# Kernel tuning notes

Measured on AMD Instinct MI355X. Metric: run time of the kernel, lower is better.

## Reference

```python
import jax, jax.numpy as jnp
import numpy as np

# Model dims
B, N, T = 2, 32, 256
D_MODEL = 128          # d_slow
D_STATE = 16
N_LAYERS = 2
EXPAND = 2
D_INNER = EXPAND * D_MODEL   # 256
D_CONV = 4
DT_RANK = (D_MODEL + 15) // 16  # 8


def setup_inputs() -> dict:
    key = jax.random.key(0)
    ks = jax.random.split(key, 8)
    s = lambda k, shape, scale: jax.random.normal(k, shape, jnp.float32) * scale
    return {
        "x": jax.random.normal(ks[0], (B, N, T, D_MODEL), jnp.float32),
        "in_proj_w": s(ks[1], (N_LAYERS, D_MODEL, 2 * D_INNER), 0.05),
        "conv_w": s(ks[2], (N_LAYERS, D_INNER, 1, D_CONV), 0.2),   # depthwise conv kernels
        "conv_b": jnp.zeros((N_LAYERS, D_INNER), jnp.float32),
        "x_proj_w": s(ks[3], (N_LAYERS, D_INNER, DT_RANK + 2 * D_STATE), 0.05),
        "dt_proj_w": s(ks[4], (N_LAYERS, DT_RANK, D_INNER), 0.1),
        "dt_proj_b": jnp.full((N_LAYERS, D_INNER), -4.0, jnp.float32),  # softplus(-4) ~ small dt
        # slow-timescale init: A_log = log(U(0.001, 0.1)) so A = -exp(A_log) is a weak decay
        "A_log": jnp.log(jax.random.uniform(ks[5], (N_LAYERS, D_INNER, D_STATE),
                                            minval=1e-3, maxval=0.1)),
        "D_param": jnp.ones((N_LAYERS, D_INNER), jnp.float32),
        "out_proj_w": s(ks[6], (N_LAYERS, D_INNER, D_MODEL), 0.05),
    }


def _selective_scan(u, delta, A, Bm, Cm, Dp):
    # u, delta: [b, t, d]; A: [d, n]; Bm, Cm: [b, t, n]; Dp: [d]
    deltaA = jnp.exp(jnp.einsum('btd,dn->btdn', delta, A))          # [b,t,d,n]
    deltaBu = jnp.einsum('btd,btn->btdn', delta * u, Bm)            # [b,t,d,n]
    # time-major for scan
    dA_t = jnp.transpose(deltaA, (1, 0, 2, 3))
    dBu_t = jnp.transpose(deltaBu, (1, 0, 2, 3))
    c_t = jnp.transpose(Cm, (1, 0, 2))

    def step(h, xs):
        dA, dBu, c = xs
        h = dA * h + dBu                                            # [b,d,n]
        y = jnp.einsum('bdn,bn->bd', h, c)
        return h, y

    h0 = jnp.zeros(u.shape[:1] + (u.shape[-1], A.shape[-1]), u.dtype)
    _, ys = jax.lax.scan(step, h0, (dA_t, dBu_t, c_t))              # ys: [t,b,d]
    y = jnp.transpose(ys, (1, 0, 2))
    return y + u * Dp


def _mamba_block(h, in_w, cw, cb, xw, dtw, dtb, A_log, Dp, ow):
    # h: [b, t, d_model]
    xz = h @ in_w                                                   # [b,t,2*d_inner]
    u, res = jnp.split(xz, 2, axis=-1)
    # causal depthwise conv over time
    u_nch = jnp.transpose(u, (0, 2, 1))                             # [b,d_inner,t]
    u_conv = jax.lax.conv_general_dilated(
        u_nch, cw, window_strides=(1,), padding=[(D_CONV - 1, 0)],
        dimension_numbers=('NCH', 'OIH', 'NCH'), feature_group_count=D_INNER)
    u = jax.nn.silu(jnp.transpose(u_conv + cb[None, :, None], (0, 2, 1)))
    # input-dependent dt, B, C
    dbl = u @ xw                                                    # [b,t,dt_rank+2n]
    dt, Bm, Cm = jnp.split(dbl, [DT_RANK, DT_RANK + D_STATE], axis=-1)
    delta = jax.nn.softplus(dt @ dtw + dtb)                         # [b,t,d_inner]
    A = -jnp.exp(A_log)                                             # [d_inner, n]
    y = _selective_scan(u, delta, A, Bm, Cm, Dp)
    return (y * jax.nn.silu(res)) @ ow


def reference(x, in_proj_w, conv_w, conv_b, x_proj_w, dt_proj_w, dt_proj_b,
              A_log, D_param, out_proj_w):
    b, n, t, d = x.shape
    h = x.reshape(b * n, t, d)
    for l in range(N_LAYERS):
        h = _mamba_block(h, in_proj_w[l], conv_w[l], conv_b[l], x_proj_w[l],
                         dt_proj_w[l], dt_proj_b[l], A_log[l], D_param[l],
                         out_proj_w[l])
    return h.reshape(b, n, t, d)
```

## Files before the change

kernel.cpp:

```cpp
#include <hip/hip_runtime.h>
#include <math.h>

#define BT 64
#define T 256
#define DM 128
#define DI 256
#define DS 16
#define DR 8
#define M_ROWS (BT*T)
#define NC 16
#define CL (T/NC)

typedef __attribute__((ext_vector_type(8))) short short8v;
typedef __attribute__((ext_vector_type(4))) float f32x4;
typedef __attribute__((ext_vector_type(4))) unsigned int uint4v;
union U8 { unsigned int u[4]; uint4v v; short8v s; };

__device__ __forceinline__ float fast_silu(float x) {
  return x * __builtin_amdgcn_rcpf(1.0f + __expf(-x));
}
__device__ __forceinline__ float softplus_f(float x) {
  return fmaxf(x, 0.0f) + __logf(1.0f + __expf(-fabsf(x)));
}

__device__ __forceinline__ void split3(const float* x, short8v& o1, short8v& o2, short8v& o3) {
  unsigned int h1[8], h2[8], h3[8];
#pragma unroll
  for (int e = 0; e < 8; e++) {
    const float xe = x[e];
    const unsigned int a = __float_as_uint(xe) & 0xFFFF0000u;
    const float r1 = xe - __uint_as_float(a);
    const unsigned int b = __float_as_uint(r1) & 0xFFFF0000u;
    const float r2 = r1 - __uint_as_float(b);
    const unsigned int c = __float_as_uint(r2) & 0xFFFF0000u;
    h1[e] = a; h2[e] = b; h3[e] = c;
  }
  U8 u1, u2, u3;
#pragma unroll
  for (int q = 0; q < 4; q++) {
    u1.u[q] = (h1[2 * q] >> 16) | (h1[2 * q + 1] & 0xFFFF0000u);
    u2.u[q] = (h2[2 * q] >> 16) | (h2[2 * q + 1] & 0xFFFF0000u);
    u3.u[q] = (h3[2 * q] >> 16) | (h3[2 * q + 1] & 0xFFFF0000u);
  }
  o1 = u1.s; o2 = u2.s; o3 = u3.s;
}

__global__ __launch_bounds__(64) void prep_all(
    const float* __restrict__ in_w, const float* __restrict__ xw,
    const float* __restrict__ dtw, const float* __restrict__ ow,
    unsigned int* __restrict__ pw1, unsigned int* __restrict__ pwb,
    unsigned int* __restrict__ pow_) {
  const int b = blockIdx.x;
  const int l = threadIdx.x;
  const int rA = l & 15, kg = l >> 4;
  float x[8];
  unsigned int* dst;
  size_t base;
  if (b < 256) {
    const int layer = b >> 7, rem = b & 127;
    const int ks = rem >> 5, cf = rem & 31;
    const int col = cf * 16 + rA, k0 = ks * 32 + kg * 8;
    const float* W = in_w + (size_t)layer * 128 * 512;
#pragma unroll
    for (int e = 0; e < 8; e++) x[e] = W[(size_t)(k0 + e) * 512 + col];
    dst = pw1 + (size_t)layer * 98304;
    base = (((size_t)ks * 32 + cf) * 64 + l) * 4;
    short8v p1, p2, p3; split3(x, p1, p2, p3);
    U8 t;
    t.s = p1; *reinterpret_cast<uint4v*>(dst + base) = t.v;
    t.s = p2; *reinterpret_cast<uint4v*>(dst + 32768 + base) = t.v;
    t.s = p3; *reinterpret_cast<uint4v*>(dst + 65536 + base) = t.v;
  } else if (b < 576) {
    const int bb = b - 256;
    const int layer = bb / 160, rem = bb % 160;
    const int ks = rem / 20, cf = rem % 20;
    const int col = cf * 16 + rA, k0 = ks * 32 + kg * 8;
    const float* xwl = xw + (size_t)layer * DI * 40;
    const float* dtwl = dtw + (size_t)layer * DR * DI;
#pragma unroll
    for (int e = 0; e < 8; e++) {
      const int k = k0 + e;
      float v = 0.f;
      if (col < 256) {
#pragma unroll
        for (int r = 0; r < DR; r++) v += xwl[k * 40 + r] * dtwl[r * DI + col];
      } else if (col < 288) {
        v = xwl[k * 40 + 8 + (col - 256)];
      }
      x[e] = v;
    }
    dst = pwb + (size_t)layer * 122880;
    base = (((size_t)ks * 20 + cf) * 64 + l) * 4;
    short8v p1, p2, p3; split3(x, p1, p2, p3);
    U8 t;
    t.s = p1; *reinterpret_cast<uint4v*>(dst + base) = t.v;
    t.s = p2; *reinterpret_cast<uint4v*>(dst + 40960 + base) = t.v;
    t.s = p3; *reinterpret_cast<uint4v*>(dst + 81920 + base) = t.v;
  } else {
    const int bb = b - 576;
    const int layer = bb >> 6, rem = bb & 63;
    const int ks = rem >> 3, cf = rem & 7;
    const int col = cf * 16 + rA, k0 = ks * 32 + kg * 8;
    const float* W = ow + (size_t)layer * 256 * 128;
#pragma unroll
    for (int e = 0; e < 8; e++) x[e] = W[(size_t)(k0 + e) * 128 + col];
    dst = pow_ + (size_t)layer * 49152;
    base = (((size_t)ks * 8 + cf) * 64 + l) * 4;
    short8v p1, p2, p3; split3(x, p1, p2, p3);
    U8 t;
    t.s = p1; *reinterpret_cast<uint4v*>(dst + base) = t.v;
    t.s = p2; *reinterpret_cast<uint4v*>(dst + 16384 + base) = t.v;
    t.s = p3; *reinterpret_cast<uint4v*>(dst + 32768 + base) = t.v;
  }
}

template <int FR, int CF, int EPI>
__global__ __launch_bounds__(256, 4) void gemm_mfma(
    const float* __restrict__ Af, const unsigned int* __restrict__ Bp,
    float* __restrict__ C, float* __restrict__ Bb, float* __restrict__ Cb,
    const float* __restrict__ dtb, int M, int Nn, int K, int cpx) {
  const int NWC = Nn / (16 * CF);
  const int tile = (blockIdx.x & 7) * cpx + (blockIdx.x >> 3);
  const int wid = tile * 4 + (threadIdx.x >> 6);
  const int l = threadIdx.x & 63;
  const int mw = wid / NWC, nw = wid % NWC;
  const int wr0 = mw * (16 * FR), wc0 = nw * (16 * CF);
  const int rA = l & 15, kg = l >> 4;
  const int NF = Nn / 16, Kt = K >> 5;

  f32x4 acc[FR][CF];
#pragma unroll
  for (int fr = 0; fr < FR; fr++)
#pragma unroll
    for (int j = 0; j < CF; j++) acc[fr][j] = (f32x4){0.f, 0.f, 0.f, 0.f};

  for (int ks = 0; ks < Kt; ks++) {
    short8v bf[3][CF];
#pragma unroll
    for (int p = 0; p < 3; p++)
#pragma unroll
      for (int j = 0; j < CF; j++) {
        U8 t;
        t.v = *reinterpret_cast<const uint4v*>(
            Bp + ((((size_t)p * Kt + ks) * NF + (wc0 >> 4) + j) * 64 + l) * 4);
        bf[p][j] = t.s;
      }
#pragma unroll
    for (int fr = 0; fr < FR; fr++) {
      const float* ap = Af + (size_t)(wr0 + fr * 16 + rA) * K + ks * 32 + kg * 8;
      float x[8];
      *reinterpret_cast<float4*>(x) = *reinterpret_cast<const float4*>(ap);
      *reinterpret_cast<float4*>(x + 4) = *reinterpret_cast<const float4*>(ap + 4);
      short8v a1, a2, a3;
      split3(x, a1, a2, a3);
#pragma unroll
      for (int j = 0; j < CF; j++) {
        f32x4 c = acc[fr][j];
        c = __builtin_amdgcn_mfma_f32_16x16x32_bf16(a1, bf[0][j], c, 0, 0, 0);
        c = __builtin_amdgcn_mfma_f32_16x16x32_bf16(a1, bf[1][j], c, 0, 0, 0);
        c = __builtin_amdgcn_mfma_f32_16x16x32_bf16(a2, bf[0][j], c, 0, 0, 0);
        c = __builtin_amdgcn_mfma_f32_16x16x32_bf16(a1, bf[2][j], c, 0, 0, 0);
        c = __builtin_amdgcn_mfma_f32_16x16x32_bf16(a3, bf[0][j], c, 0, 0, 0);
        c = __builtin_amdgcn_mfma_f32_16x16x32_bf16(a2, bf[1][j], c, 0, 0, 0);
        acc[fr][j] = c;
      }
    }
  }

  const int cr = (l >> 4) * 4;
  const int cc = l & 15;
  if (EPI == 0) {
#pragma unroll
    for (int fr = 0; fr < FR; fr++)
#pragma unroll
      for (int j = 0; j < CF; j++) {
        const int col = wc0 + j * 16 + cc;
#pragma unroll
        for (int r = 0; r < 4; r++)
          C[(size_t)(wr0 + fr * 16 + cr + r) * Nn + col] = acc[fr][j][r];
      }
  } else if (EPI == 1) {
#pragma unroll
    for (int fr = 0; fr < FR; fr++)
#pragma unroll
      for (int j = 0; j < CF; j++) {
        const int col = wc0 + j * 16 + cc;
        if (col < 256) {
          const float bias = dtb[col];
#pragma unroll
          for (int r = 0; r < 4; r++)
            C[(size_t)(wr0 + fr * 16 + cr + r) * DI + col] =
                softplus_f(acc[fr][j][r] + bias);
        } else if (col < 272) {
#pragma unroll
          for (int r = 0; r < 4; r++)
            Bb[(size_t)(wr0 + fr * 16 + cr + r) * DS + (col - 256)] = acc[fr][j][r];
        } else if (col < 288) {
#pragma unroll
          for (int r = 0; r < 4; r++)
            Cb[(size_t)(wr0 + fr * 16 + cr + r) * DS + (col - 272)] = acc[fr][j][r];
        }
      }
  } else {
#pragma unroll
    for (int fr = 0; fr < FR; fr++)
#pragma unroll
      for (int j = 0; j < CF; j++) {
        const int col = wc0 + j * 16 + cc;
        if (col < 256) {
#pragma unroll
          for (int r = 0; r < 4; r++)
            C[(size_t)(wr0 + fr * 16 + cr + r) * Nn + col] = acc[fr][j][r];
        } else {
#pragma unroll
          for (int r = 0; r < 4; r++)
            C[(size_t)(wr0 + fr * 16 + cr + r) * Nn + col] = fast_silu(acc[fr][j][r]);
        }
      }
  }
}

__global__ __launch_bounds__(256) void conv_silu_kernel(
    const float* __restrict__ xzr,
    const float* __restrict__ cw, const float* __restrict__ cb,
    float* __restrict__ u) {
  const int d = threadIdx.x;
  const int m0 = blockIdx.x * 8;
  const int t0 = m0 & (T - 1);
  const float4 cv = *reinterpret_cast<const float4*>(&cw[d * 4]);
  const float bias = cb[d];
  float w0 = 0.f, w1 = 0.f, w2 = 0.f;
  if (t0 != 0) {
    w0 = xzr[(size_t)(m0 - 3) * 512 + d];
    w1 = xzr[(size_t)(m0 - 2) * 512 + d];
    w2 = xzr[(size_t)(m0 - 1) * 512 + d];
  }
#pragma unroll
  for (int i = 0; i < 8; i++) {
    const size_t m = m0 + i;
    const float cur = xzr[m * 512 + d];
    const float a = bias + cv.x * w0 + cv.y * w1 + cv.z * w2 + cv.w * cur;
    u[m * DI + d] = fast_silu(a);
    w0 = w1; w1 = w2; w2 = cur;
  }
}

__global__ __launch_bounds__(1024) void scan_fused(
    const float* __restrict__ delta, const float* __restrict__ u,
    const float* __restrict__ Bb, const float* __restrict__ Cb,
    const float* __restrict__ xz,
    const float* __restrict__ A_log, const float* __restrict__ Dp,
    float* __restrict__ g) {
  __shared__ float sH[DS][NC][64];
  __shared__ float sS[NC][64];
  const int bt = blockIdx.x;
  const int dq = blockIdx.y;
  const int tid = threadIdx.x;
  const int c  = tid >> 6;
  const int dl = tid & 63;
  const int d  = dq * 64 + dl;

  float An[16];
  const float4* al = reinterpret_cast<const float4*>(&A_log[d * DS]);
#pragma unroll
  for (int q = 0; q < 4; q++) {
    float4 a = al[q];
    An[q * 4 + 0] = -__expf(a.x);
    An[q * 4 + 1] = -__expf(a.y);
    An[q * 4 + 2] = -__expf(a.z);
    An[q * 4 + 3] = -__expf(a.w);
  }

  float h[16];
#pragma unroll
  for (int n = 0; n < 16; n++) h[n] = 0.f;
  float Sdl = 0.f;

  const size_t m0 = (size_t)bt * T + c * CL;
  for (int t = 0; t < CL; t++) {
    const size_t m = m0 + t;
    const float dlv = delta[m * DI + d];
    const float uu = u[m * DI + d];
    const float du = dlv * uu;
    Sdl += dlv;
    const float4* bp = reinterpret_cast<const float4*>(&Bb[m * DS]);
    const float4 B0 = bp[0], B1 = bp[1], B2 = bp[2], B3 = bp[3];
    const float Bv[16] = {B0.x, B0.y, B0.z, B0.w, B1.x, B1.y, B1.z, B1.w,
                          B2.x, B2.y, B2.z, B2.w, B3.x, B3.y, B3.z, B3.w};
#pragma unroll
    for (int n = 0; n < 16; n++) {
      const float dA = __expf(dlv * An[n]);
      h[n] = dA * h[n] + du * Bv[n];
    }
  }
#pragma unroll
  for (int n = 0; n < 16; n++) sH[n][c][dl] = h[n];
  sS[c][dl] = Sdl;
  __syncthreads();

  {
    const int n2 = tid >> 6;
    const int dl2 = tid & 63;
    const int d2 = dq * 64 + dl2;
    const float An2 = -__expf(A_log[d2 * DS + n2]);
    float hin = 0.f;
#pragma unroll
    for (int cc = 0; cc < NC; cc++) {
      const float sdl = sS[cc][dl2];
      const float Hv = sH[n2][cc][dl2];
      sH[n2][cc][dl2] = hin;
      hin = __expf(An2 * sdl) * hin + Hv;
    }
  }
  __syncthreads();

#pragma unroll
  for (int n = 0; n < 16; n++) h[n] = sH[n][c][dl];
  const float Dpd = Dp[d];

  for (int t = 0; t < CL; t++) {
    const size_t m = m0 + t;
    const float dlv = delta[m * DI + d];
    const float uu = u[m * DI + d];
    const float du = dlv * uu;
    const float4* bp = reinterpret_cast<const float4*>(&Bb[m * DS]);
    const float4 B0 = bp[0], B1 = bp[1], B2 = bp[2], B3 = bp[3];
    const float4* cp = reinterpret_cast<const float4*>(&Cb[m * DS]);
    const float4 C0 = cp[0], C1 = cp[1], C2 = cp[2], C3 = cp[3];
    const float Bv[16] = {B0.x, B0.y, B0.z, B0.w, B1.x, B1.y, B1.z, B1.w,
                          B2.x, B2.y, B2.z, B2.w, B3.x, B3.y, B3.z, B3.w};
    const float Cv[16] = {C0.x, C0.y, C0.z, C0.w, C1.x, C1.y, C1.z, C1.w,
                          C2.x, C2.y, C2.z, C2.w, C3.x, C3.y, C3.z, C3.w};
    float y = 0.f;
#pragma unroll
    for (int n = 0; n < 16; n++) {
      const float dA = __expf(dlv * An[n]);
      h[n] = dA * h[n] + du * Bv[n];
      y += h[n] * Cv[n];
    }
    const float rs = xz[m * 512 + 256 + d];
    g[m * DI + d] = (y + uu * Dpd) * rs;
  }
}

extern "C" void kernel_launch(void* const* d_in, const int* in_sizes, int n_in,
                              void* d_out, int out_size, void* d_ws, size_t ws_size,
                              hipStream_t stream) {
  const float* x      = (const float*)d_in[0];
  const float* in_w   = (const float*)d_in[1];
  const float* conv_w = (const float*)d_in[2];
  const float* conv_b = (const float*)d_in[3];
  const float* xw     = (const float*)d_in[4];
  const float* dtw    = (const float*)d_in[5];
  const float* dtb    = (const float*)d_in[6];
  const float* A_log  = (const float*)d_in[7];
  const float* Dp     = (const float*)d_in[8];
  const float* ow     = (const float*)d_in[9];
  float* out = (float*)d_out;
  float* ws  = (float*)d_ws;

  float* xz = ws;
  float* u  = ws + 8388608;
  float* dg = ws + 12582912;
  float* Bb = ws + 16777216;
  float* Cb = ws + 17039360;
  float* hb = ws + 17301504;
  unsigned int* pl_w1 = (unsigned int*)(ws + 27787264);
  unsigned int* pl_wb = (unsigned int*)(ws + 27983872);
  unsigned int* pl_ow = (unsigned int*)(ws + 28229632);

  prep_all<<<704, 64, 0, stream>>>(in_w, xw, dtw, ow, pl_w1, pl_wb, pl_ow);

  for (int l = 0; l < 2; l++) {
    const float* Ain = (l == 0) ? x : hb;
    float* dst = (l == 1) ? out : hb;

    gemm_mfma<1, 4, 3><<<2048, 256, 0, stream>>>(
        Ain, pl_w1 + (size_t)l * 98304, xz,
        nullptr, nullptr, nullptr, M_ROWS, 512, 128, 256);

    conv_silu_kernel<<<M_ROWS / 8, 256, 0, stream>>>(
        xz, conv_w + (size_t)l * DI * 4, conv_b + (size_t)l * DI, u);

    gemm_mfma<1, 4, 1><<<1280, 256, 0, stream>>>(
        u, pl_wb + (size_t)l * 122880, dg, Bb, Cb, dtb + (size_t)l * DI,
        M_ROWS, 320, 256, 160);

    scan_fused<<<dim3(BT, 4), 1024, 0, stream>>>(
        dg, u, Bb, Cb, xz, A_log + (size_t)l * DI * DS, Dp + (size_t)l * DI,
        dg);

    gemm_mfma<1, 4, 0><<<512, 256, 0, stream>>>(
        dg, pl_ow + (size_t)l * 49152, dst, nullptr, nullptr, nullptr,
        M_ROWS, 128, 256, 64);
  }
}
```

Baseline: 226.0 us.

## Fold layer-0 out_proj into layer-1 in_proj and template GEMM dimensions

Precomputes the product of layer-0 out_proj and layer-1 in_proj weights (256x512) in the prep kernel. Layer 0's output projection and layer 1's input projection become a single GEMM with K=256 reading the gated scan output directly, which removes one GEMM launch and the round trip of the intermediate hidden buffer. The GEMM kernel also takes N, K and the tile stride as template constants and fully unrolls the K loop. The fused GEMM does more work per row (K=256 instead of 128), and reassociating the matrix products changes rounding slightly.

```diff
diff --git a/kernel.cpp b/kernel.cpp
--- a/kernel.cpp
+++ b/kernel.cpp
@@ -45,17 +45,25 @@
   o1 = u1.s; o2 = u2.s; o3 = u3.s;
 }
 
+__device__ __forceinline__ void store_planes(float* x, unsigned int* dst,
+                                             size_t ps, size_t base) {
+  short8v p1, p2, p3;
+  split3(x, p1, p2, p3);
+  U8 t;
+  t.s = p1; *reinterpret_cast<uint4v*>(dst + base) = t.v;
+  t.s = p2; *reinterpret_cast<uint4v*>(dst + ps + base) = t.v;
+  t.s = p3; *reinterpret_cast<uint4v*>(dst + 2 * ps + base) = t.v;
+}
+
 __global__ __launch_bounds__(64) void prep_all(
     const float* __restrict__ in_w, const float* __restrict__ xw,
     const float* __restrict__ dtw, const float* __restrict__ ow,
     unsigned int* __restrict__ pw1, unsigned int* __restrict__ pwb,
-    unsigned int* __restrict__ pow_) {
+    unsigned int* __restrict__ pow_, unsigned int* __restrict__ pwf) {
   const int b = blockIdx.x;
   const int l = threadIdx.x;
   const int rA = l & 15, kg = l >> 4;
   float x[8];
-  unsigned int* dst;
-  size_t base;
   if (b < 256) {
     const int layer = b >> 7, rem = b & 127;
     const int ks = rem >> 5, cf = rem & 31;
@@ -63,13 +71,8 @@
     const float* W = in_w + (size_t)layer * 128 * 512;
 #pragma unroll
     for (int e = 0; e < 8; e++) x[e] = W[(size_t)(k0 + e) * 512 + col];
-    dst = pw1 + (size_t)layer * 98304;
-    base = (((size_t)ks * 32 + cf) * 64 + l) * 4;
-    short8v p1, p2, p3; split3(x, p1, p2, p3);
-    U8 t;
-    t.s = p1; *reinterpret_cast<uint4v*>(dst + base) = t.v;
-    t.s = p2; *reinterpret_cast<uint4v*>(dst + 32768 + base) = t.v;
-    t.s = p3; *reinterpret_cast<uint4v*>(dst + 65536 + base) = t.v;
+    store_planes(x, pw1 + (size_t)layer * 98304, 32768,
+                 (((size_t)ks * 32 + cf) * 64 + l) * 4);
   } else if (b < 576) {
     const int bb = b - 256;
     const int layer = bb / 160, rem = bb % 160;
@@ -89,14 +92,9 @@
       }
       x[e] = v;
     }
-    dst = pwb + (size_t)layer * 122880;
-    base = (((size_t)ks * 20 + cf) * 64 + l) * 4;
-    short8v p1, p2, p3; split3(x, p1, p2, p3);
-    U8 t;
-    t.s = p1; *reinterpret_cast<uint4v*>(dst + base) = t.v;
-    t.s = p2; *reinterpret_cast<uint4v*>(dst + 40960 + base) = t.v;
-    t.s = p3; *reinterpret_cast<uint4v*>(dst + 81920 + base) = t.v;
-  } else {
+    store_planes(x, pwb + (size_t)layer * 122880, 40960,
+                 (((size_t)ks * 20 + cf) * 64 + l) * 4);
+  } else if (b < 704) {
     const int bb = b - 576;
     const int layer = bb >> 6, rem = bb & 63;
     const int ks = rem >> 3, cf = rem & 7;
@@ -104,29 +102,39 @@
     const float* W = ow + (size_t)layer * 256 * 128;
 #pragma unroll
     for (int e = 0; e < 8; e++) x[e] = W[(size_t)(k0 + e) * 128 + col];
-    dst = pow_ + (size_t)layer * 49152;
-    base = (((size_t)ks * 8 + cf) * 64 + l) * 4;
-    short8v p1, p2, p3; split3(x, p1, p2, p3);
-    U8 t;
-    t.s = p1; *reinterpret_cast<uint4v*>(dst + base) = t.v;
-    t.s = p2; *reinterpret_cast<uint4v*>(dst + 16384 + base) = t.v;
-    t.s = p3; *reinterpret_cast<uint4v*>(dst + 32768 + base) = t.v;
-  }
-}
-
-template <int FR, int CF, int EPI>
+    store_planes(x, pow_ + (size_t)layer * 49152, 16384,
+                 (((size_t)ks * 8 + cf) * 64 + l) * 4);
+  } else {
+    const int bb = b - 704;
+    const int ks = bb >> 5, cf = bb & 31;
+    const int col = cf * 16 + rA, k0 = ks * 32 + kg * 8;
+    const float* W1 = in_w + (size_t)128 * 512;
+#pragma unroll
+    for (int e = 0; e < 8; e++) {
+      const int k = k0 + e;
+      float v = 0.f;
+      for (int j = 0; j < 128; j++)
+        v = fmaf(ow[(size_t)k * 128 + j], W1[(size_t)j * 512 + col], v);
+      x[e] = v;
+    }
+    store_planes(x, pwf, 65536, (((size_t)ks * 32 + cf) * 64 + l) * 4);
+  }
+}
+
+template <int FR, int CF, int EPI, int NN, int KK, int CPX>
 __global__ __launch_bounds__(256, 4) void gemm_mfma(
     const float* __restrict__ Af, const unsigned int* __restrict__ Bp,
     float* __restrict__ C, float* __restrict__ Bb, float* __restrict__ Cb,
-    const float* __restrict__ dtb, int M, int Nn, int K, int cpx) {
-  const int NWC = Nn / (16 * CF);
-  const int tile = (blockIdx.x & 7) * cpx + (blockIdx.x >> 3);
+    const float* __restrict__ dtb, int M) {
+  constexpr int NWC = NN / (16 * CF);
+  constexpr int NF = NN / 16;
+  constexpr int Kt = KK >> 5;
+  const int tile = (blockIdx.x & 7) * CPX + (blockIdx.x >> 3);
   const int wid = tile * 4 + (threadIdx.x >> 6);
   const int l = threadIdx.x & 63;
   const int mw = wid / NWC, nw = wid % NWC;
   const int wr0 = mw * (16 * FR), wc0 = nw * (16 * CF);
   const int rA = l & 15, kg = l >> 4;
-  const int NF = Nn / 16, Kt = K >> 5;
 
   f32x4 acc[FR][CF];
 #pragma unroll
@@ -134,6 +142,7 @@
 #pragma unroll
     for (int j = 0; j < CF; j++) acc[fr][j] = (f32x4){0.f, 0.f, 0.f, 0.f};
 
+#pragma unroll
   for (int ks = 0; ks < Kt; ks++) {
     short8v bf[3][CF];
 #pragma unroll
@@ -147,7 +156,7 @@
       }
 #pragma unroll
     for (int fr = 0; fr < FR; fr++) {
-      const float* ap = Af + (size_t)(wr0 + fr * 16 + rA) * K + ks * 32 + kg * 8;
+      const float* ap = Af + (size_t)(wr0 + fr * 16 + rA) * KK + ks * 32 + kg * 8;
       float x[8];
       *reinterpret_cast<float4*>(x) = *reinterpret_cast<const float4*>(ap);
       *reinterpret_cast<float4*>(x + 4) = *reinterpret_cast<const float4*>(ap + 4);
@@ -177,7 +186,7 @@
         const int col = wc0 + j * 16 + cc;
 #pragma unroll
         for (int r = 0; r < 4; r++)
-          C[(size_t)(wr0 + fr * 16 + cr + r) * Nn + col] = acc[fr][j][r];
+          C[(size_t)(wr0 + fr * 16 + cr + r) * NN + col] = acc[fr][j][r];
       }
   } else if (EPI == 1) {
 #pragma unroll
@@ -210,11 +219,11 @@
         if (col < 256) {
 #pragma unroll
           for (int r = 0; r < 4; r++)
-            C[(size_t)(wr0 + fr * 16 + cr + r) * Nn + col] = acc[fr][j][r];
+            C[(size_t)(wr0 + fr * 16 + cr + r) * NN + col] = acc[fr][j][r];
         } else {
 #pragma unroll
           for (int r = 0; r < 4; r++)
-            C[(size_t)(wr0 + fr * 16 + cr + r) * Nn + col] = fast_silu(acc[fr][j][r]);
+            C[(size_t)(wr0 + fr * 16 + cr + r) * NN + col] = fast_silu(acc[fr][j][r]);
         }
       }
   }
@@ -364,34 +373,37 @@
   float* dg = ws + 12582912;
   float* Bb = ws + 16777216;
   float* Cb = ws + 17039360;
-  float* hb = ws + 17301504;
   unsigned int* pl_w1 = (unsigned int*)(ws + 27787264);
   unsigned int* pl_wb = (unsigned int*)(ws + 27983872);
   unsigned int* pl_ow = (unsigned int*)(ws + 28229632);
-
-  prep_all<<<704, 64, 0, stream>>>(in_w, xw, dtw, ow, pl_w1, pl_wb, pl_ow);
-
-  for (int l = 0; l < 2; l++) {
-    const float* Ain = (l == 0) ? x : hb;
-    float* dst = (l == 1) ? out : hb;
-
-    gemm_mfma<1, 4, 3><<<2048, 256, 0, stream>>>(
-        Ain, pl_w1 + (size_t)l * 98304, xz,
-        nullptr, nullptr, nullptr, M_ROWS, 512, 128, 256);
-
-    conv_silu_kernel<<<M_ROWS / 8, 256, 0, stream>>>(
-        xz, conv_w + (size_t)l * DI * 4, conv_b + (size_t)l * DI, u);
-
-    gemm_mfma<1, 4, 1><<<1280, 256, 0, stream>>>(
-        u, pl_wb + (size_t)l * 122880, dg, Bb, Cb, dtb + (size_t)l * DI,
-        M_ROWS, 320, 256, 160);
-
-    scan_fused<<<dim3(BT, 4), 1024, 0, stream>>>(
-        dg, u, Bb, Cb, xz, A_log + (size_t)l * DI * DS, Dp + (size_t)l * DI,
-        dg);
-
-    gemm_mfma<1, 4, 0><<<512, 256, 0, stream>>>(
-        dg, pl_ow + (size_t)l * 49152, dst, nullptr, nullptr, nullptr,
-        M_ROWS, 128, 256, 64);
-  }
-}
+  unsigned int* pl_wf = (unsigned int*)(ws + 28327936);
+
+  prep_all<<<960, 64, 0, stream>>>(in_w, xw, dtw, ow, pl_w1, pl_wb, pl_ow, pl_wf);
+
+  gemm_mfma<1, 4, 3, 512, 128, 256><<<2048, 256, 0, stream>>>(
+      x, pl_w1, xz, nullptr, nullptr, nullptr, M_ROWS);
+
+  conv_silu_kernel<<<M_ROWS / 8, 256, 0, stream>>>(
+      xz, conv_w, conv_b, u);
+
+  gemm_mfma<1, 4, 1, 320, 256, 160><<<1280, 256, 0, stream>>>(
+      u, pl_wb, dg, Bb, Cb, dtb, M_ROWS);
+
+  scan_fused<<<dim3(BT, 4), 1024, 0, stream>>>(
+      dg, u, Bb, Cb, xz, A_log, Dp, dg);
+
+  gemm_mfma<1, 4, 3, 512, 256, 256><<<2048, 256, 0, stream>>>(
+      dg, pl_wf, xz, nullptr, nullptr, nullptr, M_ROWS);
+
+  conv_silu_kernel<<<M_ROWS / 8, 256, 0, stream>>>(
+      xz, conv_w + DI * 4, conv_b + DI, u);
+
+  gemm_mfma<1, 4, 1, 320, 256, 160><<<1280, 256, 0, stream>>>(
+      u, pl_wb + 122880, dg, Bb, Cb, dtb + DI, M_ROWS);
+
+  scan_fused<<<dim3(BT, 4), 1024, 0, stream>>>(
+      dg, u, Bb, Cb, xz, A_log + DI * DS, Dp + DI, dg);
+
+  gemm_mfma<1, 4, 0, 128, 256, 64><<<512, 256, 0, stream>>>(
+      dg, pl_ow + 49152, out, nullptr, nullptr, nullptr, M_ROWS);
+}
```

New measurement: 243.8 us. 1.08x slower.
